# Performance work log

Measured on AMD Instinct MI355X. Metric: run time of the kernel, lower is better.

Reference implementation:

```python
import jax, jax.numpy as jnp
import numpy as np


def setup_inputs() -> dict:
    key = jax.random.key(0)
    x = jax.random.normal(key, (524288, 256), dtype=jnp.float32)
    return {"x": x}


def reference(x) -> jnp.ndarray:
    # Original builds diag(1/sqrt(diag(x^T x))) and multiplies: equivalent to
    # dividing each column by its L2 norm. Avoid the O(n*d^2) Gram matrix.
    col_sq_norm = jnp.sum(x * x, axis=0)  # [d]
    return x * jax.lax.rsqrt(col_sq_norm)  # broadcast over rows
```

## Files before the change

### kernel.cpp

```cpp
#include <hip/hip_runtime.h>

#define D   256
#define D4  64

typedef float f4 __attribute__((ext_vector_type(4)));

__global__ __launch_bounds__(256) void colsq_partial(
    const f4* __restrict__ x4, float* __restrict__ part,
    int rows, int rows_per_block) {
    __shared__ f4 red[256];
    const int t  = threadIdx.x;
    const int cg = t & 63;
    const int ro = t >> 6;
    const int r0 = blockIdx.x * rows_per_block;
    const int r1 = min(r0 + rows_per_block, rows);

    f4 acc = (f4)0.f;
    for (int r = r0 + ro; r < r1; r += 4) {
        f4 v = x4[(size_t)r * D4 + cg];
        acc += v * v;
    }
    red[t] = acc;
    __syncthreads();
    if (t < 64) {
        f4 s = red[t] + red[t + 64] + red[t + 128] + red[t + 192];
        ((f4*)part)[(size_t)blockIdx.x * D4 + t] = s;
    }
}

__global__ __launch_bounds__(256) void reduce_inv(
    const float* __restrict__ part, float* __restrict__ inv, int nb) {
    __shared__ double red[4][256];
    const int g = blockIdx.x;
    const int t = threadIdx.x;
    const f4* part4 = (const f4*)part;

    double sx = 0.0, sy = 0.0, sz = 0.0, sw = 0.0;
    for (int b = t; b < nb; b += 256) {
        f4 v = part4[(size_t)b * D4 + g];
        sx += (double)v.x; sy += (double)v.y;
        sz += (double)v.z; sw += (double)v.w;
    }
    red[0][t] = sx; red[1][t] = sy; red[2][t] = sz; red[3][t] = sw;
    __syncthreads();
    for (int ofs = 128; ofs > 0; ofs >>= 1) {
        if (t < ofs) {
            red[0][t] += red[0][t + ofs];
            red[1][t] += red[1][t + ofs];
            red[2][t] += red[2][t + ofs];
            red[3][t] += red[3][t + ofs];
        }
        __syncthreads();
    }
    if (t < 4) inv[g * 4 + t] = (float)(1.0 / sqrt(red[t][0]));
}

__global__ __launch_bounds__(256) void scale_cols(
    const f4* __restrict__ x4, const float* __restrict__ inv,
    f4* __restrict__ out4, int rows, int rows_per_block) {
    __shared__ float sinv[D];
    if (threadIdx.x < D) sinv[threadIdx.x] = inv[threadIdx.x];
    __syncthreads();
    const int t  = threadIdx.x;
    const int cg = t & 63;
    const int ro = t >> 6;
    const int r0 = blockIdx.x * rows_per_block;
    const int r1 = min(r0 + rows_per_block, rows);
    const f4 s = ((const f4*)sinv)[cg];

    const int nq = (r1 - r0 + 3) >> 2;
    for (int k = nq - 1; k >= 0; --k) {
        const int r = r0 + k * 4 + ro;
        if (r < r1) {
            const size_t idx = (size_t)r * D4 + cg;
            f4 v = x4[idx];
            __builtin_nontemporal_store(v * s, &out4[idx]);
        }
    }
}

extern "C" void kernel_launch(void* const* d_in, const int* in_sizes, int n_in,
                              void* d_out, int out_size, void* d_ws, size_t ws_size,
                              hipStream_t stream) {
    const float* x = (const float*)d_in[0];
    float* out = (float*)d_out;
    const size_t n = (size_t)in_sizes[0];
    const int rows = (int)(n / D);

    int nb = 2048;
    while (nb > 64 && ((size_t)nb * D + D) * sizeof(float) > ws_size) nb >>= 1;

    float* part = (float*)d_ws;
    float* inv  = part + (size_t)nb * D;

    const int rows_per_block = (rows + nb - 1) / nb;

    colsq_partial<<<nb, 256, 0, stream>>>((const f4*)x, part, rows, rows_per_block);
    reduce_inv<<<D4, 256, 0, stream>>>(part, inv, nb);
    scale_cols<<<nb, 256, 0, stream>>>((const f4*)x, inv, (f4*)out, rows, rows_per_block);
}
```

Measured before the change: 288.0 us.

## Fuse three column-norm kernels into one cooperative kernel with grid syncs

Replaces the partial-sum, reduce, and scale kernels with a single cooperative kernel that uses grid-wide syncs between phases. Each block keeps its own row range for both the reduction and the scaling pass, so its slice is read again in reverse order while it may still sit in cache, and two kernel launch gaps go away. The grid size is capped by occupancy so that cooperative launch is possible. In exchange it pays for two grid barriers and per-call occupancy and attribute queries on the host, and it assumes rows divide evenly by the block count.

```diff
diff --git a/kernel.cpp b/kernel.cpp
--- a/kernel.cpp
+++ b/kernel.cpp
@@ -1,81 +1,77 @@
 #include <hip/hip_runtime.h>
+#include <hip/hip_cooperative_groups.h>
+
+namespace cg = cooperative_groups;
 
 #define D   256
 #define D4  64
 
 typedef float f4 __attribute__((ext_vector_type(4)));
 
-__global__ __launch_bounds__(256) void colsq_partial(
-    const f4* __restrict__ x4, float* __restrict__ part,
-    int rows, int rows_per_block) {
-    __shared__ f4 red[256];
-    const int t  = threadIdx.x;
-    const int cg = t & 63;
-    const int ro = t >> 6;
-    const int r0 = blockIdx.x * rows_per_block;
-    const int r1 = min(r0 + rows_per_block, rows);
+__global__ __launch_bounds__(256, 8) void fused_colnorm(
+    const f4* __restrict__ x4, f4* __restrict__ out4,
+    float* __restrict__ part, float* __restrict__ inv,
+    int rows, int nb) {
+    cg::grid_group grid = cg::this_grid();
+
+    __shared__ union {
+        f4     red1[256];
+        double red2[4][256];
+    } sh;
+    __shared__ float sinv[D];
+
+    const int t   = threadIdx.x;
+    const int cgi = t & 63;
+    const int ro  = t >> 6;
+    const int b   = blockIdx.x;
+    const int rows_per_block = rows / nb;
+    const int r0 = b * rows_per_block;
+    const int r1 = r0 + rows_per_block;
 
     f4 acc = (f4)0.f;
     for (int r = r0 + ro; r < r1; r += 4) {
-        f4 v = x4[(size_t)r * D4 + cg];
+        f4 v = x4[(size_t)r * D4 + cgi];
         acc += v * v;
     }
-    red[t] = acc;
+    sh.red1[t] = acc;
     __syncthreads();
     if (t < 64) {
-        f4 s = red[t] + red[t + 64] + red[t + 128] + red[t + 192];
-        ((f4*)part)[(size_t)blockIdx.x * D4 + t] = s;
+        f4 s = sh.red1[t] + sh.red1[t + 64] + sh.red1[t + 128] + sh.red1[t + 192];
+        ((f4*)part)[(size_t)b * D4 + t] = s;
     }
-}
+    grid.sync();
 
-__global__ __launch_bounds__(256) void reduce_inv(
-    const float* __restrict__ part, float* __restrict__ inv, int nb) {
-    __shared__ double red[4][256];
-    const int g = blockIdx.x;
-    const int t = threadIdx.x;
-    const f4* part4 = (const f4*)part;
+    if (b < 64) {
+        const f4* part4 = (const f4*)part;
+        double sx = 0.0, sy = 0.0, sz = 0.0, sw = 0.0;
+        for (int i = t; i < nb; i += 256) {
+            f4 v = part4[(size_t)i * D4 + b];
+            sx += (double)v.x; sy += (double)v.y;
+            sz += (double)v.z; sw += (double)v.w;
+        }
+        sh.red2[0][t] = sx; sh.red2[1][t] = sy;
+        sh.red2[2][t] = sz; sh.red2[3][t] = sw;
+        __syncthreads();
+        for (int ofs = 128; ofs > 0; ofs >>= 1) {
+            if (t < ofs) {
+                sh.red2[0][t] += sh.red2[0][t + ofs];
+                sh.red2[1][t] += sh.red2[1][t + ofs];
+                sh.red2[2][t] += sh.red2[2][t + ofs];
+                sh.red2[3][t] += sh.red2[3][t + ofs];
+            }
+            __syncthreads();
+        }
+        if (t < 4) inv[b * 4 + t] = (float)(1.0 / sqrt(sh.red2[t][0]));
+    }
+    grid.sync();
 
-    double sx = 0.0, sy = 0.0, sz = 0.0, sw = 0.0;
-    for (int b = t; b < nb; b += 256) {
-        f4 v = part4[(size_t)b * D4 + g];
-        sx += (double)v.x; sy += (double)v.y;
-        sz += (double)v.z; sw += (double)v.w;
-    }
-    red[0][t] = sx; red[1][t] = sy; red[2][t] = sz; red[3][t] = sw;
+    if (t < D) sinv[t] = inv[t];
     __syncthreads();
-    for (int ofs = 128; ofs > 0; ofs >>= 1) {
-        if (t < ofs) {
-            red[0][t] += red[0][t + ofs];
-            red[1][t] += red[1][t + ofs];
-            red[2][t] += red[2][t + ofs];
-            red[3][t] += red[3][t + ofs];
-        }
-        __syncthreads();
-    }
-    if (t < 4) inv[g * 4 + t] = (float)(1.0 / sqrt(red[t][0]));
-}
-
-__global__ __launch_bounds__(256) void scale_cols(
-    const f4* __restrict__ x4, const float* __restrict__ inv,
-    f4* __restrict__ out4, int rows, int rows_per_block) {
-    __shared__ float sinv[D];
-    if (threadIdx.x < D) sinv[threadIdx.x] = inv[threadIdx.x];
-    __syncthreads();
-    const int t  = threadIdx.x;
-    const int cg = t & 63;
-    const int ro = t >> 6;
-    const int r0 = blockIdx.x * rows_per_block;
-    const int r1 = min(r0 + rows_per_block, rows);
-    const f4 s = ((const f4*)sinv)[cg];
-
-    const int nq = (r1 - r0 + 3) >> 2;
-    for (int k = nq - 1; k >= 0; --k) {
-        const int r = r0 + k * 4 + ro;
-        if (r < r1) {
-            const size_t idx = (size_t)r * D4 + cg;
-            f4 v = x4[idx];
-            __builtin_nontemporal_store(v * s, &out4[idx]);
-        }
+    const f4 s = ((const f4*)sinv)[cgi];
+    for (int r = r1 - 4 + ro; r >= r0; r -= 4) {
+        const size_t idx = (size_t)r * D4 + cgi;
+        f4 v = x4[idx];
+        __builtin_nontemporal_store(v * s, &out4[idx]);
     }
 }
 
@@ -87,15 +83,21 @@
     const size_t n = (size_t)in_sizes[0];
     const int rows = (int)(n / D);
 
+    int blocksPerCU = 0;
+    hipOccupancyMaxActiveBlocksPerMultiprocessor(&blocksPerCU, fused_colnorm, 256, 0);
+    int numCU = 0;
+    hipDeviceGetAttribute(&numCU, hipDeviceAttributeMultiprocessorCount, 0);
+    int maxCo = (blocksPerCU > 0 && numCU > 0) ? blocksPerCU * numCU : 2048;
+
     int nb = 2048;
-    while (nb > 64 && ((size_t)nb * D + D) * sizeof(float) > ws_size) nb >>= 1;
+    while (nb > 64 && (nb > maxCo ||
+           ((size_t)nb * D + D) * sizeof(float) > ws_size)) nb >>= 1;
 
     float* part = (float*)d_ws;
     float* inv  = part + (size_t)nb * D;
 
-    const int rows_per_block = (rows + nb - 1) / nb;
-
-    colsq_partial<<<nb, 256, 0, stream>>>((const f4*)x, part, rows, rows_per_block);
-    reduce_inv<<<D4, 256, 0, stream>>>(part, inv, nb);
-    scale_cols<<<nb, 256, 0, stream>>>((const f4*)x, inv, (f4*)out, rows, rows_per_block);
+    void* args[] = { (void*)&x, (void*)&out, (void*)&part, (void*)&inv,
+                     (void*)&rows, (void*)&nb };
+    hipLaunchCooperativeKernel((void*)fused_colnorm, dim3(nb), dim3(256),
+                               args, 0, stream);
 }
```

Measured after the change: 664.6 us. 2.31x slower.
